# Kernel tuning notes

Hardware: AMD Instinct MI355X
Metric: run time of the kernel (lower is better)

## Reference

```python
import jax, jax.numpy as jnp
import numpy as np

EPS = 1e-6


def setup_inputs() -> dict:
    key = jax.random.key(0)
    kq, kk, kv = jax.random.split(key, 3)
    B, H, S, D = 1, 16, 2048, 64
    q = jax.random.normal(kq, (B, H, S, D), dtype=jnp.float32)
    k = jax.random.normal(kk, (B, H, S, D), dtype=jnp.float32)
    v = jax.random.normal(kv, (B, H, S, D), dtype=jnp.float32)
    return {"q": q, "k": k, "v": v}


def reference(q, k, v):
    # Rebased linear attention: squared scaled QK score, causal mask,
    # normalized by running row-sum (not softmax).
    B, H, S, D = q.shape
    scale = D ** (-0.5)
    # [B,H,S,S] raw scores
    s = jnp.einsum("bhid,bhjd->bhij", q, k) * scale
    s2 = s * s
    causal = jnp.tril(jnp.ones((S, S), dtype=bool))  # k_idx <= q_idx
    s2 = jnp.where(causal, s2, jnp.zeros((), dtype=s2.dtype))
    z = jnp.sum(s2, axis=-1)  # [B,H,S]
    o = jnp.einsum("bhij,bhjd->bhid", s2, v)
    return o / (z[..., None] + EPS)
```

## Files before the change

kernel.cpp:

```cpp
#include <hip/hip_runtime.h>
#include <hip/hip_bf16.h>

typedef __attribute__((ext_vector_type(8))) short bf16x8;
typedef __attribute__((ext_vector_type(4))) short bf16x4;
typedef __attribute__((ext_vector_type(4))) float f32x4;

#define SLEN 2048
#define DDIM 64
#define KEPS 1e-6f
#define KSTR 76
#define VSTR 76

__device__ __forceinline__ short f2bf(float x) {
    unsigned u = __float_as_uint(x);
    unsigned r = (u + 0x7FFFu + ((u >> 16) & 1u)) >> 16;
    return (short)r;
}

__device__ __forceinline__ unsigned cvtpk(float lo, float hi) {
    unsigned r;
    asm("v_cvt_pk_bf16_f32 %0, %1, %2" : "=v"(r) : "v"(lo), "v"(hi));
    return r;
}

__device__ __forceinline__ f32x4 mfma16x16x32bf16(bf16x8 a, bf16x8 b, f32x4 c) {
#if __has_builtin(__builtin_amdgcn_mfma_f32_16x16x32_bf16)
    return __builtin_amdgcn_mfma_f32_16x16x32_bf16(a, b, c, 0, 0, 0);
#else
    asm("v_mfma_f32_16x16x32_bf16 %0, %1, %2, %0" : "+v"(c) : "v"(a), "v"(b));
    return c;
#endif
}

__device__ __forceinline__ f32x4 mfma16x16x16bf16(bf16x4 a, bf16x4 b, f32x4 c) {
#if __has_builtin(__builtin_amdgcn_mfma_f32_16x16x16bf16_1k)
    return __builtin_amdgcn_mfma_f32_16x16x16bf16_1k(a, b, c, 0, 0, 0);
#else
    asm("v_mfma_f32_16x16x16_bf16 %0, %1, %2, %0" : "+v"(c) : "v"(a), "v"(b));
    return c;
#endif
}

__global__ void __launch_bounds__(512, 4) rebased_attn_kernel(
    const float* __restrict__ Q, const float* __restrict__ K,
    const float* __restrict__ V, float* __restrict__ O)
{
    __shared__ __align__(16) short Klds[2][2][64 * KSTR];
    __shared__ __align__(16) short VTlds[2][2][64 * VSTR];

    const int b    = blockIdx.x;
    const int half = b >> 8;
    const int r8   = b & 255;
    const int h    = (half << 3) | (r8 >> 5);
    const int g    = half ? (31 - (r8 & 31)) : (r8 & 31);

    const int tid  = threadIdx.x;
    const int w    = tid >> 6;
    const int lane = tid & 63;
    const int l15  = lane & 15;
    const int lg   = lane >> 4;
    const int qt   = w & 3;
    const int p    = w >> 2;

    const int q0 = g * 64 + qt * 16;

    const float* __restrict__ Qh = Q + (size_t)h * SLEN * DDIM;
    const float* __restrict__ Kh = K + (size_t)h * SLEN * DDIM;
    const float* __restrict__ Vh = V + (size_t)h * SLEN * DDIM;
    float* __restrict__ Oh = O + (size_t)h * SLEN * DDIM;

    bf16x8 qf[2];
#pragma unroll
    for (int f = 0; f < 2; ++f) {
        const float* src = Qh + (size_t)(q0 + l15) * DDIM + 32 * f + lg * 8;
        float4 a = *reinterpret_cast<const float4*>(src);
        float4 c = *reinterpret_cast<const float4*>(src + 4);
        bf16x8 v;
        v[0] = f2bf(a.x); v[1] = f2bf(a.y); v[2] = f2bf(a.z); v[3] = f2bf(a.w);
        v[4] = f2bf(c.x); v[5] = f2bf(c.y); v[6] = f2bf(c.z); v[7] = f2bf(c.w);
        qf[f] = v;
    }

    f32x4 oacc[4];
#pragma unroll
    for (int nb = 0; nb < 4; ++nb) oacc[nb] = (f32x4){0.f, 0.f, 0.f, 0.f};
    float zacc = 0.f;

    const int pt   = tid >> 8;
    const int t255 = tid & 255;
    const int ksr  = t255 >> 4;
    const int ksc  = (t255 & 15) * 4;
    const int vj0  = (t255 >> 4) * 4;

    const int T = (g + 2) >> 1;

    float4 kreg[4], vreg[4];
    {
        const int base = pt * 64;
#pragma unroll
        for (int q = 0; q < 4; ++q)
            kreg[q] = *reinterpret_cast<const float4*>(Kh + (size_t)(base + q * 16 + ksr) * DDIM + ksc);
#pragma unroll
        for (int r = 0; r < 4; ++r)
            vreg[r] = *reinterpret_cast<const float4*>(Vh + (size_t)(base + vj0 + r) * DDIM + ksc);
#pragma unroll
        for (int q = 0; q < 4; ++q) {
            uint2 pk = make_uint2(cvtpk(kreg[q].x, kreg[q].y), cvtpk(kreg[q].z, kreg[q].w));
            *reinterpret_cast<uint2*>(&Klds[0][pt][(q * 16 + ksr) * KSTR + ksc]) = pk;
        }
#pragma unroll
        for (int c = 0; c < 4; ++c) {
            uint2 pk = make_uint2(
                cvtpk(((const float*)&vreg[0])[c], ((const float*)&vreg[1])[c]),
                cvtpk(((const float*)&vreg[2])[c], ((const float*)&vreg[3])[c]));
            *reinterpret_cast<uint2*>(&VTlds[0][pt][(ksc + c) * VSTR + vj0]) = pk;
        }
    }
    __syncthreads();

    for (int t = 0; t < T; ++t) {
        const int  cur     = t & 1;
        const bool hasNext = (t < T - 1);

        if (hasNext) {
            const int base = (2 * (t + 1) + pt) * 64;
#pragma unroll
            for (int q = 0; q < 4; ++q)
                kreg[q] = *reinterpret_cast<const float4*>(Kh + (size_t)(base + q * 16 + ksr) * DDIM + ksc);
#pragma unroll
            for (int r = 0; r < 4; ++r)
                vreg[r] = *reinterpret_cast<const float4*>(Vh + (size_t)(base + vj0 + r) * DDIM + ksc);
        }

        const int kt = 2 * t + p;
        if (kt <= g) {
            const bool diag = (kt == g);
            const int  nsub = diag ? (qt + 1) : 4;
            __builtin_amdgcn_s_setprio(1);
            for (int js = 0; js < nsub; ++js) {
                const short* kb = &Klds[cur][p][(js * 16 + l15) * KSTR + lg * 8];
                bf16x4 k00 = *reinterpret_cast<const bf16x4*>(kb);
                bf16x4 k01 = *reinterpret_cast<const bf16x4*>(kb + 4);
                bf16x4 k10 = *reinterpret_cast<const bf16x4*>(kb + 32);
                bf16x4 k11 = *reinterpret_cast<const bf16x4*>(kb + 36);
                bf16x8 kf0 = __builtin_shufflevector(k00, k01, 0, 1, 2, 3, 4, 5, 6, 7);
                bf16x8 kf1 = __builtin_shufflevector(k10, k11, 0, 1, 2, 3, 4, 5, 6, 7);

                f32x4 sacc = (f32x4){0.f, 0.f, 0.f, 0.f};
                sacc = mfma16x16x32bf16(kf0, qf[0], sacc);
                sacc = mfma16x16x32bf16(kf1, qf[1], sacc);

                float pv[4];
#pragma unroll
                for (int rr = 0; rr < 4; ++rr)
                    pv[rr] = sacc[rr] * sacc[rr] * 0.015625f;
                if (diag && js == qt) {
#pragma unroll
                    for (int rr = 0; rr < 4; ++rr)
                        if (lg * 4 + rr > l15) pv[rr] = 0.f;
                }
                zacc += (pv[0] + pv[1]) + (pv[2] + pv[3]);

                uint2 pu = make_uint2(cvtpk(pv[0], pv[1]), cvtpk(pv[2], pv[3]));
                bf16x4 pfr = *reinterpret_cast<bf16x4*>(&pu);
#pragma unroll
                for (int nb = 0; nb < 4; ++nb) {
                    bf16x4 vf = *reinterpret_cast<const bf16x4*>(
                        &VTlds[cur][p][(nb * 16 + l15) * VSTR + js * 16 + lg * 4]);
                    oacc[nb] = mfma16x16x16bf16(pfr, vf, oacc[nb]);
                }
            }
            __builtin_amdgcn_s_setprio(0);
        }

        if (hasNext) {
            const int nxt = cur ^ 1;
#pragma unroll
            for (int q = 0; q < 4; ++q) {
                uint2 pk = make_uint2(cvtpk(kreg[q].x, kreg[q].y), cvtpk(kreg[q].z, kreg[q].w));
                *reinterpret_cast<uint2*>(&Klds[nxt][pt][(q * 16 + ksr) * KSTR + ksc]) = pk;
            }
#pragma unroll
            for (int c = 0; c < 4; ++c) {
                uint2 pk = make_uint2(
                    cvtpk(((const float*)&vreg[0])[c], ((const float*)&vreg[1])[c]),
                    cvtpk(((const float*)&vreg[2])[c], ((const float*)&vreg[3])[c]));
                *reinterpret_cast<uint2*>(&VTlds[nxt][pt][(ksc + c) * VSTR + vj0]) = pk;
            }
        }
        __syncthreads();
    }

    float* red = (float*)&Klds[0][0][0];
    if (p == 1) {
        const int idx = (qt * 64 + lane) * 17;
#pragma unroll
        for (int nb = 0; nb < 4; ++nb)
#pragma unroll
            for (int rr = 0; rr < 4; ++rr)
                red[idx + nb * 4 + rr] = oacc[nb][rr];
        red[idx + 16] = zacc;
    }
    __syncthreads();
    if (p == 0) {
        const int idx = (qt * 64 + lane) * 17;
#pragma unroll
        for (int nb = 0; nb < 4; ++nb)
#pragma unroll
            for (int rr = 0; rr < 4; ++rr)
                oacc[nb][rr] += red[idx + nb * 4 + rr];
        zacc += red[idx + 16];

        float z = zacc;
        z += __shfl_xor(z, 16);
        z += __shfl_xor(z, 32);

#pragma unroll
        for (int rr = 0; rr < 4; ++rr) {
            float zi  = __shfl(z, lg * 4 + rr);
            float inv = 1.f / (zi + KEPS);
            int row   = q0 + lg * 4 + rr;
#pragma unroll
            for (int nb = 0; nb < 4; ++nb) {
                Oh[(size_t)row * DDIM + nb * 16 + l15] = oacc[nb][rr] * inv;
            }
        }
    }
}

extern "C" void kernel_launch(void* const* d_in, const int* in_sizes, int n_in,
                              void* d_out, int out_size, void* d_ws, size_t ws_size,
                              hipStream_t stream) {
    const float* q = (const float*)d_in[0];
    const float* k = (const float*)d_in[1];
    const float* v = (const float*)d_in[2];
    float* o = (float*)d_out;
    hipLaunchKernelGGL(rebased_attn_kernel, dim3(512), dim3(512), 0, stream, q, k, v, o);
}
```

Baseline: 34.99 us.

## Pair complementary causal query tiles per block to share K/V tile loads

Each block now handles two query tiles, g and 31-g, so every block does balanced causal work and each K/V tile staged in LDS is reused by both query sets. Grid drops to 256 blocks, and the block-to-head mapping is arranged around the XCD index. LDS stride shrinks to 72, the K fragment loads become single 16-byte reads, and Q conversion uses packed cvt. The cost is higher register pressure (launch bounds relaxed to 2 blocks), fewer blocks in flight, and a separate reduction buffer in LDS.

```diff
diff --git a/kernel.cpp b/kernel.cpp
--- a/kernel.cpp
+++ b/kernel.cpp
@@ -8,14 +8,7 @@
 #define SLEN 2048
 #define DDIM 64
 #define KEPS 1e-6f
-#define KSTR 76
-#define VSTR 76
-
-__device__ __forceinline__ short f2bf(float x) {
-    unsigned u = __float_as_uint(x);
-    unsigned r = (u + 0x7FFFu + ((u >> 16) & 1u)) >> 16;
-    return (short)r;
-}
+#define STR 72
 
 __device__ __forceinline__ unsigned cvtpk(float lo, float hi) {
     unsigned r;
@@ -23,7 +16,7 @@
     return r;
 }
 
-__device__ __forceinline__ f32x4 mfma16x16x32bf16(bf16x8 a, bf16x8 b, f32x4 c) {
+__device__ __forceinline__ f32x4 mfma32(bf16x8 a, bf16x8 b, f32x4 c) {
 #if __has_builtin(__builtin_amdgcn_mfma_f32_16x16x32_bf16)
     return __builtin_amdgcn_mfma_f32_16x16x32_bf16(a, b, c, 0, 0, 0);
 #else
@@ -32,7 +25,7 @@
 #endif
 }
 
-__device__ __forceinline__ f32x4 mfma16x16x16bf16(bf16x4 a, bf16x4 b, f32x4 c) {
+__device__ __forceinline__ f32x4 mfma16(bf16x4 a, bf16x4 b, f32x4 c) {
 #if __has_builtin(__builtin_amdgcn_mfma_f32_16x16x16bf16_1k)
     return __builtin_amdgcn_mfma_f32_16x16x16bf16_1k(a, b, c, 0, 0, 0);
 #else
@@ -41,60 +34,79 @@
 #endif
 }
 
-__global__ void __launch_bounds__(512, 4) rebased_attn_kernel(
+__global__ void __launch_bounds__(512, 2) rebased_attn_kernel(
     const float* __restrict__ Q, const float* __restrict__ K,
     const float* __restrict__ V, float* __restrict__ O)
 {
-    __shared__ __align__(16) short Klds[2][2][64 * KSTR];
-    __shared__ __align__(16) short VTlds[2][2][64 * VSTR];
-
-    const int b    = blockIdx.x;
-    const int half = b >> 8;
-    const int r8   = b & 255;
-    const int h    = (half << 3) | (r8 >> 5);
-    const int g    = half ? (31 - (r8 & 31)) : (r8 & 31);
+    __shared__ __align__(16) short Klds[2][2][64 * STR];
+    __shared__ __align__(16) short VTlds[2][2][64 * STR];
+    __shared__ float red[4][64][34];
+
+    const int bid  = blockIdx.x;
+    const int xcd  = bid & 7;
+    const int slot = bid >> 3;
+    const int gg   = slot & 15;
+    const int h    = ((slot >> 4) << 3) | xcd;
+
+    const int g1 = gg;
+    const int g2 = 31 - gg;
 
     const int tid  = threadIdx.x;
     const int w    = tid >> 6;
     const int lane = tid & 63;
     const int l15  = lane & 15;
     const int lg   = lane >> 4;
-    const int qt   = w & 3;
+    const int qw   = w & 3;
     const int p    = w >> 2;
 
-    const int q0 = g * 64 + qt * 16;
+    const int q1 = g1 * 64 + qw * 16;
+    const int q2 = g2 * 64 + qw * 16;
 
     const float* __restrict__ Qh = Q + (size_t)h * SLEN * DDIM;
     const float* __restrict__ Kh = K + (size_t)h * SLEN * DDIM;
     const float* __restrict__ Vh = V + (size_t)h * SLEN * DDIM;
     float* __restrict__ Oh = O + (size_t)h * SLEN * DDIM;
 
-    bf16x8 qf[2];
+    bf16x8 qf1[2], qf2[2];
 #pragma unroll
     for (int f = 0; f < 2; ++f) {
-        const float* src = Qh + (size_t)(q0 + l15) * DDIM + 32 * f + lg * 8;
-        float4 a = *reinterpret_cast<const float4*>(src);
-        float4 c = *reinterpret_cast<const float4*>(src + 4);
-        bf16x8 v;
-        v[0] = f2bf(a.x); v[1] = f2bf(a.y); v[2] = f2bf(a.z); v[3] = f2bf(a.w);
-        v[4] = f2bf(c.x); v[5] = f2bf(c.y); v[6] = f2bf(c.z); v[7] = f2bf(c.w);
-        qf[f] = v;
-    }
-
-    f32x4 oacc[4];
-#pragma unroll
-    for (int nb = 0; nb < 4; ++nb) oacc[nb] = (f32x4){0.f, 0.f, 0.f, 0.f};
-    float zacc = 0.f;
+        {
+            const float* src = Qh + (size_t)(q1 + l15) * DDIM + 32 * f + lg * 8;
+            float4 a = *reinterpret_cast<const float4*>(src);
+            float4 c = *reinterpret_cast<const float4*>(src + 4);
+            uint4 u = make_uint4(cvtpk(a.x, a.y), cvtpk(a.z, a.w),
+                                 cvtpk(c.x, c.y), cvtpk(c.z, c.w));
+            qf1[f] = *reinterpret_cast<bf16x8*>(&u);
+        }
+        {
+            const float* src = Qh + (size_t)(q2 + l15) * DDIM + 32 * f + lg * 8;
+            float4 a = *reinterpret_cast<const float4*>(src);
+            float4 c = *reinterpret_cast<const float4*>(src + 4);
+            uint4 u = make_uint4(cvtpk(a.x, a.y), cvtpk(a.z, a.w),
+                                 cvtpk(c.x, c.y), cvtpk(c.z, c.w));
+            qf2[f] = *reinterpret_cast<bf16x8*>(&u);
+        }
+    }
+
+    f32x4 o1[4], o2[4];
+#pragma unroll
+    for (int nb = 0; nb < 4; ++nb) {
+        o1[nb] = (f32x4){0.f, 0.f, 0.f, 0.f};
+        o2[nb] = (f32x4){0.f, 0.f, 0.f, 0.f};
+    }
+    float z1 = 0.f, z2 = 0.f;
 
     const int pt   = tid >> 8;
     const int t255 = tid & 255;
     const int ksr  = t255 >> 4;
     const int ksc  = (t255 & 15) * 4;
-    const int vj0  = (t255 >> 4) * 4;
-
-    const int T = (g + 2) >> 1;
+    const int vr0  = (t255 & 15) * 4;
+    const int vc0  = (t255 >> 4) * 4;
+
+    const int T = (g2 + 2) >> 1;
 
     float4 kreg[4], vreg[4];
+
     {
         const int base = pt * 64;
 #pragma unroll
@@ -102,18 +114,18 @@
             kreg[q] = *reinterpret_cast<const float4*>(Kh + (size_t)(base + q * 16 + ksr) * DDIM + ksc);
 #pragma unroll
         for (int r = 0; r < 4; ++r)
-            vreg[r] = *reinterpret_cast<const float4*>(Vh + (size_t)(base + vj0 + r) * DDIM + ksc);
+            vreg[r] = *reinterpret_cast<const float4*>(Vh + (size_t)(base + vr0 + r) * DDIM + vc0);
 #pragma unroll
         for (int q = 0; q < 4; ++q) {
             uint2 pk = make_uint2(cvtpk(kreg[q].x, kreg[q].y), cvtpk(kreg[q].z, kreg[q].w));
-            *reinterpret_cast<uint2*>(&Klds[0][pt][(q * 16 + ksr) * KSTR + ksc]) = pk;
+            *reinterpret_cast<uint2*>(&Klds[0][pt][(q * 16 + ksr) * STR + ksc]) = pk;
         }
 #pragma unroll
         for (int c = 0; c < 4; ++c) {
             uint2 pk = make_uint2(
                 cvtpk(((const float*)&vreg[0])[c], ((const float*)&vreg[1])[c]),
                 cvtpk(((const float*)&vreg[2])[c], ((const float*)&vreg[3])[c]));
-            *reinterpret_cast<uint2*>(&VTlds[0][pt][(ksc + c) * VSTR + vj0]) = pk;
+            *reinterpret_cast<uint2*>(&VTlds[0][pt][(vc0 + c) * STR + vr0]) = pk;
         }
     }
     __syncthreads();
@@ -129,45 +141,58 @@
                 kreg[q] = *reinterpret_cast<const float4*>(Kh + (size_t)(base + q * 16 + ksr) * DDIM + ksc);
 #pragma unroll
             for (int r = 0; r < 4; ++r)
-                vreg[r] = *reinterpret_cast<const float4*>(Vh + (size_t)(base + vj0 + r) * DDIM + ksc);
+                vreg[r] = *reinterpret_cast<const float4*>(Vh + (size_t)(base + vr0 + r) * DDIM + vc0);
         }
 
         const int kt = 2 * t + p;
-        if (kt <= g) {
-            const bool diag = (kt == g);
-            const int  nsub = diag ? (qt + 1) : 4;
+        if (kt <= g2) {
+            const int nsub = (kt == g2) ? (qw + 1) : 4;
             __builtin_amdgcn_s_setprio(1);
             for (int js = 0; js < nsub; ++js) {
-                const short* kb = &Klds[cur][p][(js * 16 + l15) * KSTR + lg * 8];
-                bf16x4 k00 = *reinterpret_cast<const bf16x4*>(kb);
-                bf16x4 k01 = *reinterpret_cast<const bf16x4*>(kb + 4);
-                bf16x4 k10 = *reinterpret_cast<const bf16x4*>(kb + 32);
-                bf16x4 k11 = *reinterpret_cast<const bf16x4*>(kb + 36);
-                bf16x8 kf0 = __builtin_shufflevector(k00, k01, 0, 1, 2, 3, 4, 5, 6, 7);
-                bf16x8 kf1 = __builtin_shufflevector(k10, k11, 0, 1, 2, 3, 4, 5, 6, 7);
-
-                f32x4 sacc = (f32x4){0.f, 0.f, 0.f, 0.f};
-                sacc = mfma16x16x32bf16(kf0, qf[0], sacc);
-                sacc = mfma16x16x32bf16(kf1, qf[1], sacc);
-
-                float pv[4];
-#pragma unroll
-                for (int rr = 0; rr < 4; ++rr)
-                    pv[rr] = sacc[rr] * sacc[rr] * 0.015625f;
-                if (diag && js == qt) {
+                const short* kp = &Klds[cur][p][(js * 16 + l15) * STR + lg * 8];
+                bf16x8 kf0 = *reinterpret_cast<const bf16x8*>(kp);
+                bf16x8 kf1 = *reinterpret_cast<const bf16x8*>(kp + 32);
+
+                f32x4 s2 = (f32x4){0.f, 0.f, 0.f, 0.f};
+                s2 = mfma32(kf0, qf2[0], s2);
+                s2 = mfma32(kf1, qf2[1], s2);
+                float p2[4];
+#pragma unroll
+                for (int rr = 0; rr < 4; ++rr) p2[rr] = s2[rr] * s2[rr] * 0.015625f;
+                if (kt == g2 && js == qw) {
 #pragma unroll
                     for (int rr = 0; rr < 4; ++rr)
-                        if (lg * 4 + rr > l15) pv[rr] = 0.f;
+                        if (lg * 4 + rr > l15) p2[rr] = 0.f;
                 }
-                zacc += (pv[0] + pv[1]) + (pv[2] + pv[3]);
-
-                uint2 pu = make_uint2(cvtpk(pv[0], pv[1]), cvtpk(pv[2], pv[3]));
-                bf16x4 pfr = *reinterpret_cast<bf16x4*>(&pu);
+                z2 += (p2[0] + p2[1]) + (p2[2] + p2[3]);
+                uint2 pu2 = make_uint2(cvtpk(p2[0], p2[1]), cvtpk(p2[2], p2[3]));
+                bf16x4 pf2 = *reinterpret_cast<bf16x4*>(&pu2);
+
+                const bool a1 = (kt < g1) || (kt == g1 && js <= qw);
+                bf16x4 pf1 = pf2;
+                if (a1) {
+                    f32x4 s1 = (f32x4){0.f, 0.f, 0.f, 0.f};
+                    s1 = mfma32(kf0, qf1[0], s1);
+                    s1 = mfma32(kf1, qf1[1], s1);
+                    float p1[4];
+#pragma unroll
+                    for (int rr = 0; rr < 4; ++rr) p1[rr] = s1[rr] * s1[rr] * 0.015625f;
+                    if (kt == g1 && js == qw) {
+#pragma unroll
+                        for (int rr = 0; rr < 4; ++rr)
+                            if (lg * 4 + rr > l15) p1[rr] = 0.f;
+                    }
+                    z1 += (p1[0] + p1[1]) + (p1[2] + p1[3]);
+                    uint2 pu1 = make_uint2(cvtpk(p1[0], p1[1]), cvtpk(p1[2], p1[3]));
+                    pf1 = *reinterpret_cast<bf16x4*>(&pu1);
+                }
+
 #pragma unroll
                 for (int nb = 0; nb < 4; ++nb) {
                     bf16x4 vf = *reinterpret_cast<const bf16x4*>(
-                        &VTlds[cur][p][(nb * 16 + l15) * VSTR + js * 16 + lg * 4]);
-                    oacc[nb] = mfma16x16x16bf16(pfr, vf, oacc[nb]);
+                        &VTlds[cur][p][(nb * 16 + l15) * STR + js * 16 + lg * 4]);
+                    o2[nb] = mfma16(pf2, vf, o2[nb]);
+                    if (a1) o1[nb] = mfma16(pf1, vf, o1[nb]);
                 }
             }
             __builtin_amdgcn_s_setprio(0);
@@ -178,51 +203,59 @@
 #pragma unroll
             for (int q = 0; q < 4; ++q) {
                 uint2 pk = make_uint2(cvtpk(kreg[q].x, kreg[q].y), cvtpk(kreg[q].z, kreg[q].w));
-                *reinterpret_cast<uint2*>(&Klds[nxt][pt][(q * 16 + ksr) * KSTR + ksc]) = pk;
+                *reinterpret_cast<uint2*>(&Klds[nxt][pt][(q * 16 + ksr) * STR + ksc]) = pk;
             }
 #pragma unroll
             for (int c = 0; c < 4; ++c) {
                 uint2 pk = make_uint2(
                     cvtpk(((const float*)&vreg[0])[c], ((const float*)&vreg[1])[c]),
                     cvtpk(((const float*)&vreg[2])[c], ((const float*)&vreg[3])[c]));
-                *reinterpret_cast<uint2*>(&VTlds[nxt][pt][(ksc + c) * VSTR + vj0]) = pk;
+                *reinterpret_cast<uint2*>(&VTlds[nxt][pt][(vc0 + c) * STR + vr0]) = pk;
             }
         }
         __syncthreads();
     }
 
-    float* red = (float*)&Klds[0][0][0];
     if (p == 1) {
-        const int idx = (qt * 64 + lane) * 17;
+        float* r = &red[qw][lane][0];
 #pragma unroll
         for (int nb = 0; nb < 4; ++nb)
 #pragma unroll
-            for (int rr = 0; rr < 4; ++rr)
-                red[idx + nb * 4 + rr] = oacc[nb][rr];
-        red[idx + 16] = zacc;
+            for (int rr = 0; rr < 4; ++rr) {
+                r[nb * 4 + rr]      = o2[nb][rr];
+                r[17 + nb * 4 + rr] = o1[nb][rr];
+            }
+        r[16] = z2;
+        r[33] = z1;
     }
     __syncthreads();
     if (p == 0) {
-        const int idx = (qt * 64 + lane) * 17;
+        const float* r = &red[qw][lane][0];
 #pragma unroll
         for (int nb = 0; nb < 4; ++nb)
 #pragma unroll
-            for (int rr = 0; rr < 4; ++rr)
-                oacc[nb][rr] += red[idx + nb * 4 + rr];
-        zacc += red[idx + 16];
-
-        float z = zacc;
-        z += __shfl_xor(z, 16);
-        z += __shfl_xor(z, 32);
+            for (int rr = 0; rr < 4; ++rr) {
+                o2[nb][rr] += r[nb * 4 + rr];
+                o1[nb][rr] += r[17 + nb * 4 + rr];
+            }
+        z2 += r[16];
+        z1 += r[33];
+
+        z2 += __shfl_xor(z2, 16); z2 += __shfl_xor(z2, 32);
+        z1 += __shfl_xor(z1, 16); z1 += __shfl_xor(z1, 32);
 
 #pragma unroll
         for (int rr = 0; rr < 4; ++rr) {
-            float zi  = __shfl(z, lg * 4 + rr);
-            float inv = 1.f / (zi + KEPS);
-            int row   = q0 + lg * 4 + rr;
+            float zi2 = __shfl(z2, lg * 4 + rr);
+            float zi1 = __shfl(z1, lg * 4 + rr);
+            float i2 = 1.f / (zi2 + KEPS);
+            float i1 = 1.f / (zi1 + KEPS);
+            const int r2 = q2 + lg * 4 + rr;
+            const int r1 = q1 + lg * 4 + rr;
 #pragma unroll
             for (int nb = 0; nb < 4; ++nb) {
-                Oh[(size_t)row * DDIM + nb * 16 + l15] = oacc[nb][rr] * inv;
+                Oh[(size_t)r2 * DDIM + nb * 16 + l15] = o2[nb][rr] * i2;
+                Oh[(size_t)r1 * DDIM + nb * 16 + l15] = o1[nb][rr] * i1;
             }
         }
     }
@@ -235,5 +268,5 @@
     const float* k = (const float*)d_in[1];
     const float* v = (const float*)d_in[2];
     float* o = (float*)d_out;
-    hipLaunchKernelGGL(rebased_attn_kernel, dim3(512), dim3(512), 0, stream, q, k, v, o);
-}
+    hipLaunchKernelGGL(rebased_attn_kernel, dim3(256), dim3(512), 0, stream, q, k, v, o);
+}
```

Result: slower. 41.39 us (+18.3%).

## Pre-convert K and transposed V to bf16, use 1024-thread blocks

Applied to the files above, without the earlier changes.

A separate prep kernel converts K to bf16 and V to a transposed bf16 layout in the workspace, so the attention kernel loads half the bytes and copies them straight into LDS without any conversion. Blocks grow to 16 waves that split the key tiles four ways instead of two, with a three-way reduction at the end. Block-to-head mapping is changed to group heads by XCD and to pair causal tiles for load balance. The cost is an extra kernel launch, an extra round trip of K/V through memory, and a single-buffered LDS with two barriers per step instead of double buffering.

```diff
diff --git a/kernel.cpp b/kernel.cpp
--- a/kernel.cpp
+++ b/kernel.cpp
@@ -7,9 +7,9 @@
 
 #define SLEN 2048
 #define DDIM 64
+#define NH 16
 #define KEPS 1e-6f
-#define KSTR 76
-#define VSTR 76
+#define STR 72
 
 __device__ __forceinline__ short f2bf(float x) {
     unsigned u = __float_as_uint(x);
@@ -23,7 +23,7 @@
     return r;
 }
 
-__device__ __forceinline__ f32x4 mfma16x16x32bf16(bf16x8 a, bf16x8 b, f32x4 c) {
+__device__ __forceinline__ f32x4 mfma32(bf16x8 a, bf16x8 b, f32x4 c) {
 #if __has_builtin(__builtin_amdgcn_mfma_f32_16x16x32_bf16)
     return __builtin_amdgcn_mfma_f32_16x16x32_bf16(a, b, c, 0, 0, 0);
 #else
@@ -32,7 +32,7 @@
 #endif
 }
 
-__device__ __forceinline__ f32x4 mfma16x16x16bf16(bf16x4 a, bf16x4 b, f32x4 c) {
+__device__ __forceinline__ f32x4 mfma16(bf16x4 a, bf16x4 b, f32x4 c) {
 #if __has_builtin(__builtin_amdgcn_mfma_f32_16x16x16bf16_1k)
     return __builtin_amdgcn_mfma_f32_16x16x16bf16_1k(a, b, c, 0, 0, 0);
 #else
@@ -41,33 +41,73 @@
 #endif
 }
 
-__global__ void __launch_bounds__(512, 4) rebased_attn_kernel(
-    const float* __restrict__ Q, const float* __restrict__ K,
-    const float* __restrict__ V, float* __restrict__ O)
+__global__ void __launch_bounds__(256) prep_kernel(
+    const float* __restrict__ K, const float* __restrict__ V,
+    short* __restrict__ Kb, short* __restrict__ VTb)
 {
-    __shared__ __align__(16) short Klds[2][2][64 * KSTR];
-    __shared__ __align__(16) short VTlds[2][2][64 * VSTR];
-
-    const int b    = blockIdx.x;
-    const int half = b >> 8;
-    const int r8   = b & 255;
-    const int h    = (half << 3) | (r8 >> 5);
-    const int g    = half ? (31 - (r8 & 31)) : (r8 & 31);
+    __shared__ short vt[64 * STR];
+    const int b   = blockIdx.x;
+    const int h   = b >> 5;
+    const int jt  = b & 31;
+    const int t   = threadIdx.x;
+    const int r   = t >> 2;
+    const int c0  = (t & 3) * 16;
+    const int row = jt * 64 + r;
+
+    {
+        const float4* src = (const float4*)(K + ((size_t)h * SLEN + row) * DDIM + c0);
+        float4 a = src[0], bq = src[1], cq = src[2], dq = src[3];
+        uint4 o0 = make_uint4(cvtpk(a.x, a.y), cvtpk(a.z, a.w), cvtpk(bq.x, bq.y), cvtpk(bq.z, bq.w));
+        uint4 o1 = make_uint4(cvtpk(cq.x, cq.y), cvtpk(cq.z, cq.w), cvtpk(dq.x, dq.y), cvtpk(dq.z, dq.w));
+        uint4* dst = (uint4*)(Kb + ((size_t)h * SLEN + row) * DDIM + c0);
+        dst[0] = o0; dst[1] = o1;
+    }
+    {
+        const float4* src = (const float4*)(V + ((size_t)h * SLEN + row) * DDIM + c0);
+        float4 a = src[0], bq = src[1], cq = src[2], dq = src[3];
+        float f[16] = {a.x,a.y,a.z,a.w, bq.x,bq.y,bq.z,bq.w, cq.x,cq.y,cq.z,cq.w, dq.x,dq.y,dq.z,dq.w};
+#pragma unroll
+        for (int c = 0; c < 16; ++c)
+            vt[(c0 + c) * STR + r] = f2bf(f[c]);
+    }
+    __syncthreads();
+    {
+        const int d = r, j0 = c0;
+        const short* s = &vt[d * STR + j0];
+        uint4 o0 = *(const uint4*)s;
+        uint4 o1 = *(const uint4*)(s + 8);
+        uint4* dst = (uint4*)(VTb + ((size_t)h * DDIM + d) * SLEN + jt * 64 + j0);
+        dst[0] = o0; dst[1] = o1;
+    }
+}
+
+template<bool BSRC>
+__device__ __forceinline__ void attn_body(
+    const float* __restrict__ Q, const void* __restrict__ Ksrc,
+    const void* __restrict__ Vsrc, float* __restrict__ O)
+{
+    __shared__ __align__(16) short smem[2][4][64 * STR];
+
+    const int bid = blockIdx.x;
+    const int xcd = bid & 7;
+    const int u   = bid >> 3;
+    const int hb  = u & 1;
+    const int jj  = u >> 1;
+    const int h   = (hb << 3) | xcd;
+    const int g   = (jj < 16) ? jj : 47 - jj;
 
     const int tid  = threadIdx.x;
     const int w    = tid >> 6;
     const int lane = tid & 63;
     const int l15  = lane & 15;
     const int lg   = lane >> 4;
-    const int qt   = w & 3;
+    const int qw   = w & 3;
     const int p    = w >> 2;
 
-    const int q0 = g * 64 + qt * 16;
-
-    const float* __restrict__ Qh = Q + (size_t)h * SLEN * DDIM;
-    const float* __restrict__ Kh = K + (size_t)h * SLEN * DDIM;
-    const float* __restrict__ Vh = V + (size_t)h * SLEN * DDIM;
-    float* __restrict__ Oh = O + (size_t)h * SLEN * DDIM;
+    const int q0 = g * 64 + qw * 16;
+
+    const float* Qh = Q + (size_t)h * SLEN * DDIM;
+    float* Oh = O + (size_t)h * SLEN * DDIM;
 
     bf16x8 qf[2];
 #pragma unroll
@@ -75,10 +115,8 @@
         const float* src = Qh + (size_t)(q0 + l15) * DDIM + 32 * f + lg * 8;
         float4 a = *reinterpret_cast<const float4*>(src);
         float4 c = *reinterpret_cast<const float4*>(src + 4);
-        bf16x8 v;
-        v[0] = f2bf(a.x); v[1] = f2bf(a.y); v[2] = f2bf(a.z); v[3] = f2bf(a.w);
-        v[4] = f2bf(c.x); v[5] = f2bf(c.y); v[6] = f2bf(c.z); v[7] = f2bf(c.w);
-        qf[f] = v;
+        uint4 uq = make_uint4(cvtpk(a.x, a.y), cvtpk(a.z, a.w), cvtpk(c.x, c.y), cvtpk(c.z, c.w));
+        qf[f] = *reinterpret_cast<bf16x8*>(&uq);
     }
 
     f32x4 oacc[4];
@@ -86,75 +124,87 @@
     for (int nb = 0; nb < 4; ++nb) oacc[nb] = (f32x4){0.f, 0.f, 0.f, 0.f};
     float zacc = 0.f;
 
-    const int pt   = tid >> 8;
     const int t255 = tid & 255;
-    const int ksr  = t255 >> 4;
-    const int ksc  = (t255 & 15) * 4;
-    const int vj0  = (t255 >> 4) * 4;
-
-    const int T = (g + 2) >> 1;
-
+    const int sr = t255 >> 2;
+    const int sc = (t255 & 3) * 16;
+    const int ksr = t255 >> 4, ksc = (t255 & 15) * 4;
+    const int vr0 = (t255 & 15) * 4, vc0 = (t255 >> 4) * 4;
+
+    const short* Kb  = (const short*)Ksrc;
+    const short* VTb = (const short*)Vsrc;
+    const float* Kf  = (const float*)Ksrc;
+    const float* Vf  = (const float*)Vsrc;
+
+    uint4 ka0, ka1, va0, va1;
     float4 kreg[4], vreg[4];
-    {
-        const int base = pt * 64;
-#pragma unroll
-        for (int q = 0; q < 4; ++q)
-            kreg[q] = *reinterpret_cast<const float4*>(Kh + (size_t)(base + q * 16 + ksr) * DDIM + ksc);
-#pragma unroll
-        for (int r = 0; r < 4; ++r)
-            vreg[r] = *reinterpret_cast<const float4*>(Vh + (size_t)(base + vj0 + r) * DDIM + ksc);
-#pragma unroll
-        for (int q = 0; q < 4; ++q) {
-            uint2 pk = make_uint2(cvtpk(kreg[q].x, kreg[q].y), cvtpk(kreg[q].z, kreg[q].w));
-            *reinterpret_cast<uint2*>(&Klds[0][pt][(q * 16 + ksr) * KSTR + ksc]) = pk;
-        }
-#pragma unroll
-        for (int c = 0; c < 4; ++c) {
-            uint2 pk = make_uint2(
-                cvtpk(((const float*)&vreg[0])[c], ((const float*)&vreg[1])[c]),
-                cvtpk(((const float*)&vreg[2])[c], ((const float*)&vreg[3])[c]));
-            *reinterpret_cast<uint2*>(&VTlds[0][pt][(ksc + c) * VSTR + vj0]) = pk;
-        }
-    }
+
+    auto issue_loads = [&](int kt) {
+        if (BSRC) {
+            const uint4* kg = (const uint4*)(Kb + ((size_t)h * SLEN + kt * 64 + sr) * DDIM + sc);
+            ka0 = kg[0]; ka1 = kg[1];
+            const uint4* vg = (const uint4*)(VTb + ((size_t)h * DDIM + sr) * SLEN + kt * 64 + sc);
+            va0 = vg[0]; va1 = vg[1];
+        } else {
+            const int base = kt * 64;
+#pragma unroll
+            for (int q = 0; q < 4; ++q)
+                kreg[q] = *reinterpret_cast<const float4*>(Kf + ((size_t)h * SLEN + base + q * 16 + ksr) * DDIM + ksc);
+#pragma unroll
+            for (int r = 0; r < 4; ++r)
+                vreg[r] = *reinterpret_cast<const float4*>(Vf + ((size_t)h * SLEN + base + vr0 + r) * DDIM + vc0);
+        }
+    };
+    auto write_lds = [&]() {
+        if (BSRC) {
+            short* kd = &smem[0][p][sr * STR + sc];
+            *(uint4*)kd = ka0; *(uint4*)(kd + 8) = ka1;
+            short* vd = &smem[1][p][sr * STR + sc];
+            *(uint4*)vd = va0; *(uint4*)(vd + 8) = va1;
+        } else {
+#pragma unroll
+            for (int q = 0; q < 4; ++q) {
+                uint2 pk = make_uint2(cvtpk(kreg[q].x, kreg[q].y), cvtpk(kreg[q].z, kreg[q].w));
+                *reinterpret_cast<uint2*>(&smem[0][p][(q * 16 + ksr) * STR + ksc]) = pk;
+            }
+#pragma unroll
+            for (int c = 0; c < 4; ++c) {
+                uint2 pk = make_uint2(
+                    cvtpk(((const float*)&vreg[0])[c], ((const float*)&vreg[1])[c]),
+                    cvtpk(((const float*)&vreg[2])[c], ((const float*)&vreg[3])[c]));
+                *reinterpret_cast<uint2*>(&smem[1][p][(vc0 + c) * STR + vr0]) = pk;
+            }
+        }
+    };
+
+    const int T = (g >> 2) + 1;
+
+    if (p <= g) { issue_loads(p); write_lds(); }
     __syncthreads();
 
     for (int t = 0; t < T; ++t) {
-        const int  cur     = t & 1;
-        const bool hasNext = (t < T - 1);
-
-        if (hasNext) {
-            const int base = (2 * (t + 1) + pt) * 64;
-#pragma unroll
-            for (int q = 0; q < 4; ++q)
-                kreg[q] = *reinterpret_cast<const float4*>(Kh + (size_t)(base + q * 16 + ksr) * DDIM + ksc);
-#pragma unroll
-            for (int r = 0; r < 4; ++r)
-                vreg[r] = *reinterpret_cast<const float4*>(Vh + (size_t)(base + vj0 + r) * DDIM + ksc);
-        }
-
-        const int kt = 2 * t + p;
+        const int kt  = 4 * t + p;
+        const int nxt = kt + 4;
+
+        if (nxt <= g) issue_loads(nxt);
+
         if (kt <= g) {
-            const bool diag = (kt == g);
-            const int  nsub = diag ? (qt + 1) : 4;
+            const bool dodiag = (kt == g);
+            const int  nsub   = dodiag ? (qw + 1) : 4;
             __builtin_amdgcn_s_setprio(1);
             for (int js = 0; js < nsub; ++js) {
-                const short* kb = &Klds[cur][p][(js * 16 + l15) * KSTR + lg * 8];
-                bf16x4 k00 = *reinterpret_cast<const bf16x4*>(kb);
-                bf16x4 k01 = *reinterpret_cast<const bf16x4*>(kb + 4);
-                bf16x4 k10 = *reinterpret_cast<const bf16x4*>(kb + 32);
-                bf16x4 k11 = *reinterpret_cast<const bf16x4*>(kb + 36);
-                bf16x8 kf0 = __builtin_shufflevector(k00, k01, 0, 1, 2, 3, 4, 5, 6, 7);
-                bf16x8 kf1 = __builtin_shufflevector(k10, k11, 0, 1, 2, 3, 4, 5, 6, 7);
+                const short* kp = &smem[0][p][(js * 16 + l15) * STR + lg * 8];
+                bf16x8 kf0 = *reinterpret_cast<const bf16x8*>(kp);
+                bf16x8 kf1 = *reinterpret_cast<const bf16x8*>(kp + 32);
 
                 f32x4 sacc = (f32x4){0.f, 0.f, 0.f, 0.f};
-                sacc = mfma16x16x32bf16(kf0, qf[0], sacc);
-                sacc = mfma16x16x32bf16(kf1, qf[1], sacc);
+                sacc = mfma32(kf0, qf[0], sacc);
+                sacc = mfma32(kf1, qf[1], sacc);
 
                 float pv[4];
 #pragma unroll
                 for (int rr = 0; rr < 4; ++rr)
                     pv[rr] = sacc[rr] * sacc[rr] * 0.015625f;
-                if (diag && js == qt) {
+                if (dodiag && js == qw) {
 #pragma unroll
                     for (int rr = 0; rr < 4; ++rr)
                         if (lg * 4 + rr > l15) pv[rr] = 0.f;
@@ -166,50 +216,43 @@
 #pragma unroll
                 for (int nb = 0; nb < 4; ++nb) {
                     bf16x4 vf = *reinterpret_cast<const bf16x4*>(
-                        &VTlds[cur][p][(nb * 16 + l15) * VSTR + js * 16 + lg * 4]);
-                    oacc[nb] = mfma16x16x16bf16(pfr, vf, oacc[nb]);
+                        &smem[1][p][(nb * 16 + l15) * STR + js * 16 + lg * 4]);
+                    oacc[nb] = mfma16(pfr, vf, oacc[nb]);
                 }
             }
             __builtin_amdgcn_s_setprio(0);
         }
 
-        if (hasNext) {
-            const int nxt = cur ^ 1;
-#pragma unroll
-            for (int q = 0; q < 4; ++q) {
-                uint2 pk = make_uint2(cvtpk(kreg[q].x, kreg[q].y), cvtpk(kreg[q].z, kreg[q].w));
-                *reinterpret_cast<uint2*>(&Klds[nxt][pt][(q * 16 + ksr) * KSTR + ksc]) = pk;
-            }
-#pragma unroll
-            for (int c = 0; c < 4; ++c) {
-                uint2 pk = make_uint2(
-                    cvtpk(((const float*)&vreg[0])[c], ((const float*)&vreg[1])[c]),
-                    cvtpk(((const float*)&vreg[2])[c], ((const float*)&vreg[3])[c]));
-                *reinterpret_cast<uint2*>(&VTlds[nxt][pt][(ksc + c) * VSTR + vj0]) = pk;
-            }
-        }
-        __syncthreads();
-    }
-
-    float* red = (float*)&Klds[0][0][0];
-    if (p == 1) {
-        const int idx = (qt * 64 + lane) * 17;
+        if (t + 1 < T) {
+            __syncthreads();
+            if (nxt <= g) write_lds();
+            __syncthreads();
+        }
+    }
+
+    __syncthreads();
+    float* red = (float*)smem;
+    if (p != 0) {
+        float* r = &red[(((p - 1) * 4 + qw) * 64 + lane) * 17];
 #pragma unroll
         for (int nb = 0; nb < 4; ++nb)
 #pragma unroll
             for (int rr = 0; rr < 4; ++rr)
-                red[idx + nb * 4 + rr] = oacc[nb][rr];
-        red[idx + 16] = zacc;
+                r[nb * 4 + rr] = oacc[nb][rr];
+        r[16] = zacc;
     }
     __syncthreads();
     if (p == 0) {
-        const int idx = (qt * 64 + lane) * 17;
-#pragma unroll
-        for (int nb = 0; nb < 4; ++nb)
-#pragma unroll
-            for (int rr = 0; rr < 4; ++rr)
-                oacc[nb][rr] += red[idx + nb * 4 + rr];
-        zacc += red[idx + 16];
+#pragma unroll
+        for (int pp = 1; pp < 4; ++pp) {
+            const float* r = &red[(((pp - 1) * 4 + qw) * 64 + lane) * 17];
+#pragma unroll
+            for (int nb = 0; nb < 4; ++nb)
+#pragma unroll
+                for (int rr = 0; rr < 4; ++rr)
+                    oacc[nb][rr] += r[nb * 4 + rr];
+            zacc += r[16];
+        }
 
         float z = zacc;
         z += __shfl_xor(z, 16);
@@ -219,13 +262,26 @@
         for (int rr = 0; rr < 4; ++rr) {
             float zi  = __shfl(z, lg * 4 + rr);
             float inv = 1.f / (zi + KEPS);
-            int row   = q0 + lg * 4 + rr;
-#pragma unroll
-            for (int nb = 0; nb < 4; ++nb) {
+            const int row = q0 + lg * 4 + rr;
+#pragma unroll
+            for (int nb = 0; nb < 4; ++nb)
                 Oh[(size_t)row * DDIM + nb * 16 + l15] = oacc[nb][rr] * inv;
-            }
-        }
-    }
+        }
+    }
+}
+
+__global__ void __launch_bounds__(1024, 8) attn_bf16(
+    const float* __restrict__ Q, const short* __restrict__ Kb,
+    const short* __restrict__ VTb, float* __restrict__ O)
+{
+    attn_body<true>(Q, Kb, VTb, O);
+}
+
+__global__ void __launch_bounds__(1024, 4) attn_fp32(
+    const float* __restrict__ Q, const float* __restrict__ K,
+    const float* __restrict__ V, float* __restrict__ O)
+{
+    attn_body<false>(Q, K, V, O);
 }
 
 extern "C" void kernel_launch(void* const* d_in, const int* in_sizes, int n_in,
@@ -235,5 +291,16 @@
     const float* k = (const float*)d_in[1];
     const float* v = (const float*)d_in[2];
     float* o = (float*)d_out;
-    hipLaunchKernelGGL(rebased_attn_kernel, dim3(512), dim3(512), 0, stream, q, k, v, o);
-}
+
+    const size_t elems = (size_t)NH * SLEN * DDIM;
+    const size_t need  = 2 * elems * sizeof(short);
+
+    if (ws_size >= need) {
+        short* Kb  = (short*)d_ws;
+        short* VTb = Kb + elems;
+        hipLaunchKernelGGL(prep_kernel, dim3(512), dim3(256), 0, stream, k, v, Kb, VTb);
+        hipLaunchKernelGGL(attn_bf16, dim3(512), dim3(1024), 0, stream, q, Kb, VTb, o);
+    } else {
+        hipLaunchKernelGGL(attn_fp32, dim3(512), dim3(1024), 0, stream, q, k, v, o);
+    }
+}
```

After: 39.36 us. 1.13x slower.
